# Kernel tuning notes

Hardware: AMD Instinct MI355X
Metric: run time of the kernel (lower is better)

## Reference

```python
import jax, jax.numpy as jnp
import numpy as np

N_NODES = 100000
N_EDGES = 1600000
IN_DIM = 165
HIDDEN = 128
OUT_DIM = 2


def gcn_conv(x, W, b, src, dst, n_nodes):
    """PyG GCNConv: h = x @ W; add self-loops; sym-normalized scatter-add; + bias."""
    h = x @ W  # [N, F_out]
    loop = jnp.arange(n_nodes, dtype=src.dtype)
    src_f = jnp.concatenate([src, loop])  # [E + N]
    dst_f = jnp.concatenate([dst, loop])
    deg = jax.ops.segment_sum(jnp.ones(src_f.shape[0], dtype=h.dtype), dst_f,
                              num_segments=n_nodes)  # in-degree incl. self-loop
    dinv = jnp.where(deg > 0, jax.lax.rsqrt(deg), jnp.zeros_like(deg))
    norm = dinv[src_f] * dinv[dst_f]  # [E + N]
    msg = h[src_f] * norm[:, None]  # gather + scale, [E+N, F_out]
    out = jax.ops.segment_sum(msg, dst_f, num_segments=n_nodes)  # scatter-add
    return out + b


def setup_inputs() -> dict:
    key = jax.random.key(0)
    k_x, k_e, k_w1, k_b1, k_w2, k_b2 = jax.random.split(key, 6)
    x = jax.random.normal(k_x, (N_NODES, IN_DIM), dtype=jnp.float32)
    edge_index = jax.random.randint(k_e, (2, N_EDGES), 0, N_NODES, dtype=jnp.int64)
    # Glorot-like init for linear weights, zeros for bias (PyG defaults)
    W1 = jax.random.normal(k_w1, (IN_DIM, HIDDEN), dtype=jnp.float32) / np.sqrt(IN_DIM)
    b1 = jnp.zeros((HIDDEN,), dtype=jnp.float32)
    W2 = jax.random.normal(k_w2, (HIDDEN, OUT_DIM), dtype=jnp.float32) / np.sqrt(HIDDEN)
    b2 = jnp.zeros((OUT_DIM,), dtype=jnp.float32)
    return {"x": x, "edge_index": edge_index, "W1": W1, "b1": b1, "W2": W2, "b2": b2}


def reference(x, edge_index, W1, b1, W2, b2):
    src, dst = edge_index[0], edge_index[1]
    h = gcn_conv(x, W1, b1, src, dst, N_NODES)
    h = jax.nn.relu(h)
    # dropout: eval mode (training=False) -> identity
    out = gcn_conv(h, W2, b2, src, dst, N_NODES)
    return out
```

## Files before the change

kernel.cpp:

```cpp
#include <hip/hip_runtime.h>
#include <hip/hip_fp16.h>

#define N_NODES 100000
#define N_EDGES 1600000
#define IN_DIM  165
#define HIDDEN  128
#define OUT_DIM 2

#define NBKT 196
#define CHUNK 4096
#define NCHUNK ((N_EDGES + CHUNK - 1) / CHUNK)
#define PADCAP 10240
#define KPAD 176
#define GROWS 64
#define XSTRIDE 176

typedef _Float16 half8_t __attribute__((ext_vector_type(8)));
typedef _Float16 half4_t __attribute__((ext_vector_type(4)));
typedef float floatx4 __attribute__((ext_vector_type(4)));


__global__ __launch_bounds__(512) void k_part2(const int* __restrict__ src,
                                               const int* __restrict__ dst,
                                               int* __restrict__ bcnt,
                                               unsigned* __restrict__ arena) {
    __shared__ int hist[256];
    __shared__ int gbase[256];

    int t = threadIdx.x;
    int e0 = blockIdx.x * CHUNK;
    int nE = N_EDGES - e0; if (nE > CHUNK) nE = CHUNK;
    int n4 = nE >> 2;
    const int4* dst4 = (const int4*)(dst + e0);
    const int4* src4 = (const int4*)(src + e0);

    if (t < 256) hist[t] = 0;
    __syncthreads();

    for (int i = t; i < n4; i += 512) {
        int4 d = dst4[i];
        atomicAdd(&hist[d.x >> 9], 1);
        atomicAdd(&hist[d.y >> 9], 1);
        atomicAdd(&hist[d.z >> 9], 1);
        atomicAdd(&hist[d.w >> 9], 1);
    }
    __syncthreads();

    if (t < NBKT) gbase[t] = t * PADCAP + atomicAdd(&bcnt[t], hist[t]);
    if (t < 256) hist[t] = 0;
    __syncthreads();

    for (int i = t; i < n4; i += 512) {
        int4 d = dst4[i];
        int4 s = src4[i];
        #pragma unroll
        for (int j = 0; j < 4; j++) {
            int dd = (j == 0) ? d.x : (j == 1) ? d.y : (j == 2) ? d.z : d.w;
            int ss = (j == 0) ? s.x : (j == 1) ? s.y : (j == 2) ? s.z : s.w;
            int bk = dd >> 9;
            unsigned entry = (unsigned)ss | ((unsigned)(dd & 511) << 17);
            int idx = atomicAdd(&hist[bk], 1);
            arena[gbase[bk] + idx] = entry;
        }
    }
}


__global__ __launch_bounds__(1024) void k_sort4(const unsigned* __restrict__ arena,
                                                const int* __restrict__ bcnt,
                                                int* __restrict__ csr,
                                                int* __restrict__ rowstart,
                                                int* __restrict__ rowend,
                                                float* __restrict__ dinv) {
    __shared__ int cnt[512];
    __shared__ int cur[512];
    __shared__ int wsum[4];
    int b = blockIdx.x;
    int n0 = b << 9;
    int t = threadIdx.x;
    int lane = t & 63, wid = t >> 6;
    int total = bcnt[b];
    int abase = b * PADCAP;
    int dbase = b * PADCAP;
    int nt4 = total >> 2;
    const uint4* arena4 = (const uint4*)(arena + abase);

    if (t < 512) cnt[t] = 0;
    __syncthreads();
    for (int p = t; p < nt4; p += 1024) {
        uint4 e = arena4[p];
        atomicAdd(&cnt[e.x >> 17], 1);
        atomicAdd(&cnt[e.y >> 17], 1);
        atomicAdd(&cnt[e.z >> 17], 1);
        atomicAdd(&cnt[e.w >> 17], 1);
    }
    {
        int p = (nt4 << 2) + t;
        if (p < total) atomicAdd(&cnt[arena[abase + p] >> 17], 1);
    }
    __syncthreads();

    int c0 = 0, c1 = 0, s = 0, inc = 0;
    if (t < 256) {
        c0 = cnt[2 * t];
        c1 = cnt[2 * t + 1];
        s = c0 + c1;
        inc = s;
        #pragma unroll
        for (int off = 1; off < 64; off <<= 1) {
            int y = __shfl_up(inc, off);
            if (lane >= off) inc += y;
        }
        if (lane == 63) wsum[wid] = inc;
    }
    __syncthreads();
    if (t == 0) {
        int acc = 0;
        #pragma unroll
        for (int w = 0; w < 4; w++) { int tv = wsum[w]; wsum[w] = acc; acc += tv; }
    }
    __syncthreads();
    if (t < 256) {
        int base = dbase + wsum[wid] + (inc - s);
        cur[2 * t] = base;
        cur[2 * t + 1] = base + c0;
        int node0 = n0 + 2 * t;
        if (node0 < N_NODES) {
            rowstart[node0] = base;
            rowend[node0] = base + c0;
            dinv[node0] = rsqrtf((float)(c0 + 1));
        }
        if (node0 + 1 < N_NODES) {
            rowstart[node0 + 1] = base + c0;
            rowend[node0 + 1] = base + c0 + c1;
            dinv[node0 + 1] = rsqrtf((float)(c1 + 1));
        }
    }
    __syncthreads();

    for (int p = t; p < nt4; p += 1024) {
        uint4 e = arena4[p];
        #pragma unroll
        for (int j = 0; j < 4; j++) {
            unsigned entry = (j == 0) ? e.x : (j == 1) ? e.y : (j == 2) ? e.z : e.w;
            int local = (int)(entry >> 17);
            int sv = (int)(entry & 0x1FFFFu);
            int pos = atomicAdd(&cur[local], 1);
            csr[pos] = sv;
        }
    }
    {
        int p = (nt4 << 2) + t;
        if (p < total) {
            unsigned entry = arena[abase + p];
            int local = (int)(entry >> 17);
            int sv = (int)(entry & 0x1FFFFu);
            int pos = atomicAdd(&cur[local], 1);
            csr[pos] = sv;
        }
    }
}


__global__ void k_w1t(const float* __restrict__ W1, _Float16* __restrict__ w1t,
                      int* __restrict__ bcnt) {
    if (blockIdx.x == 0 && threadIdx.x < NBKT) bcnt[threadIdx.x] = 0;
    int idx = blockIdx.x * 256 + threadIdx.x;
    if (idx < HIDDEN * KPAD) {
        int c = idx / KPAD, k = idx - c * KPAD;
        float v = (k < IN_DIM) ? W1[k * HIDDEN + c] : 0.f;
        w1t[idx] = (_Float16)v;
    }
}


__global__ __launch_bounds__(256, 8) void k_gemm1(const float* __restrict__ x,
                                                  const _Float16* __restrict__ w1t,
                                                  const float* __restrict__ dinv,
                                                  _Float16* __restrict__ h1s) {
    __shared__ __align__(16) _Float16 xs[GROWS * XSTRIDE];
    int t = threadIdx.x;
    int wid = t >> 6, lane = t & 63;
    int row0 = blockIdx.x * GROWS;
    int nrows = N_NODES - row0; if (nrows > GROWS) nrows = GROWS;
    int nflt = nrows * IN_DIM;

    const float4* xb4 = (const float4*)(x + (size_t)row0 * IN_DIM);
    int n4 = nflt >> 2;
    for (int i = t; i < n4; i += 256) {
        float4 v = xb4[i];
        int e = i << 2;
        #pragma unroll
        for (int j = 0; j < 4; j++) {
            int ee = e + j;
            int r = ee / IN_DIM;
            int c = ee - r * IN_DIM;
            float f = (j == 0) ? v.x : (j == 1) ? v.y : (j == 2) ? v.z : v.w;
            xs[(r * XSTRIDE + c) ^ ((r & 7) << 3)] = (_Float16)f;
        }
    }
    for (int i = t; i < GROWS * (XSTRIDE - IN_DIM); i += 256) {
        int r = i / (XSTRIDE - IN_DIM);
        int c = IN_DIM + (i - r * (XSTRIDE - IN_DIM));
        xs[(r * XSTRIDE + c) ^ ((r & 7) << 3)] = (_Float16)0.f;
    }
    __syncthreads();

    int mrow = wid * 16;
    if (mrow >= nrows) return;
    int m = lane & 15;
    int quad = lane >> 4;
    int rbase = (mrow + m) * XSTRIDE;
    int sm = (m & 7) << 3;
    int grow = row0 + mrow;

    floatx4 acc[8];
    #pragma unroll
    for (int i = 0; i < 8; i++) acc[i] = (floatx4)(0.f);

    #pragma unroll
    for (int kc = 0; kc < 5; kc++) {
        int kb = kc * 32 + quad * 8;
        half8_t a = *(const half8_t*)&xs[(rbase + kb) ^ sm];
        #pragma unroll
        for (int cb = 0; cb < 8; cb++) {
            int col = cb * 16 + m;
            half8_t bf = *(const half8_t*)&w1t[col * KPAD + kb];
            acc[cb] = __builtin_amdgcn_mfma_f32_16x16x32_f16(a, bf, acc[cb], 0, 0, 0);
        }
    }
    {
        int kb = 160 + quad * 4;
        half4_t a = *(const half4_t*)&xs[(rbase + kb) ^ sm];
        #pragma unroll
        for (int cb = 0; cb < 8; cb++) {
            int col = cb * 16 + m;
            half4_t bf = *(const half4_t*)&w1t[col * KPAD + kb];
            acc[cb] = __builtin_amdgcn_mfma_f32_16x16x16f16(a, bf, acc[cb], 0, 0, 0);
        }
    }
    float dv[4];
    #pragma unroll
    for (int r = 0; r < 4; r++) dv[r] = dinv[grow + quad * 4 + r];
    #pragma unroll
    for (int cb = 0; cb < 8; cb++) {
        #pragma unroll
        for (int r = 0; r < 4; r++) {
            h1s[(size_t)(grow + quad * 4 + r) * HIDDEN + cb * 16 + m] =
                (_Float16)(acc[cb][r] * dv[r]);
        }
    }
}


__global__ __launch_bounds__(256) void k_agg1(const _Float16* __restrict__ h1,
                                              const int* __restrict__ rowstart,
                                              const int* __restrict__ rowend,
                                              const int* __restrict__ csr,
                                              const float* __restrict__ dinv,
                                              const float* __restrict__ b1,
                                              const float* __restrict__ W2,
                                              float2* __restrict__ h2s,
                                              int nodeoff) {
    int wid = threadIdx.x >> 6, lane = threadIdx.x & 63;
    int el = lane & 15;
    int es = lane >> 4;
    int node = nodeoff + blockIdx.x * 4 + wid;

    float acc[8];
    {
        half8_t v = *(const half8_t*)(h1 + (size_t)node * HIDDEN + el * 8);
        #pragma unroll
        for (int j = 0; j < 8; j++) acc[j] = (es == 0) ? (float)v[j] : 0.f;
    }

    int p0 = rowstart[node], p1 = rowend[node];
    int p = p0 + es;
    for (; p + 4 < p1; p += 8) {
        int sA = csr[p];
        int sB = csr[p + 4];
        half8_t vA = *(const half8_t*)(h1 + (size_t)sA * HIDDEN + el * 8);
        half8_t vB = *(const half8_t*)(h1 + (size_t)sB * HIDDEN + el * 8);
        #pragma unroll
        for (int j = 0; j < 8; j++) acc[j] += (float)vA[j];
        #pragma unroll
        for (int j = 0; j < 8; j++) acc[j] += (float)vB[j];
    }
    if (p < p1) {
        int s = csr[p];
        half8_t v = *(const half8_t*)(h1 + (size_t)s * HIDDEN + el * 8);
        #pragma unroll
        for (int j = 0; j < 8; j++) acc[j] += (float)v[j];
    }

    #pragma unroll
    for (int j = 0; j < 8; j++) {
        acc[j] += __shfl_xor(acc[j], 16);
        acc[j] += __shfl_xor(acc[j], 32);
    }

    float di = dinv[node];
    float4 bb0 = ((const float4*)b1)[el * 2];
    float4 bb1 = ((const float4*)b1)[el * 2 + 1];
    float bv[8] = {bb0.x, bb0.y, bb0.z, bb0.w, bb1.x, bb1.y, bb1.z, bb1.w};
    float a0 = 0.f, a1 = 0.f;
    #pragma unroll
    for (int j = 0; j < 8; j++) {
        float z = fmaf(di, acc[j], bv[j]);
        float r = fmaxf(z, 0.f);
        float2 w = ((const float2*)W2)[el * 8 + j];
        a0 = fmaf(r, w.x, a0);
        a1 = fmaf(r, w.y, a1);
    }
    #pragma unroll
    for (int off = 8; off; off >>= 1) {
        a0 += __shfl_xor(a0, off);
        a1 += __shfl_xor(a1, off);
    }
    if (lane == 0) h2s[node] = make_float2(di * a0, di * a1);
}


__global__ __launch_bounds__(256) void k_agg2(const float2* __restrict__ h2s,
                                              const int* __restrict__ rowstart,
                                              const int* __restrict__ rowend,
                                              const int* __restrict__ csr,
                                              const float* __restrict__ dinv,
                                              const float* __restrict__ b2,
                                              float2* __restrict__ out) {
    int wid = threadIdx.x >> 6, lane = threadIdx.x & 63;
    int sub = lane >> 4, el = lane & 15;
    int node = blockIdx.x * 16 + wid * 4 + sub;
    int p0 = rowstart[node], p1 = rowend[node];
    float ax = 0.f, ay = 0.f;
    for (int p = p0 + el; p < p1; p += 16) {
        float2 g = h2s[csr[p]];
        ax += g.x;
        ay += g.y;
    }
    #pragma unroll
    for (int off = 8; off; off >>= 1) {
        ax += __shfl_xor(ax, off);
        ay += __shfl_xor(ay, off);
    }
    if (el == 0) {
        float2 self = h2s[node];
        float di = dinv[node];
        out[node] = make_float2(fmaf(di, self.x + ax, b2[0]),
                                fmaf(di, self.y + ay, b2[1]));
    }
}


extern "C" void kernel_launch(void* const* d_in, const int* in_sizes, int n_in,
                              void* d_out, int out_size, void* d_ws, size_t ws_size,
                              hipStream_t stream) {
    const float* x  = (const float*)d_in[0];
    const int*   ei = (const int*)d_in[1];
    const float* W1 = (const float*)d_in[2];
    const float* b1 = (const float*)d_in[3];
    const float* W2 = (const float*)d_in[4];
    const float* b2 = (const float*)d_in[5];
    float* out = (float*)d_out;

    const int* src = ei;
    const int* dst = ei + N_EDGES;

    char* ws = (char*)d_ws;
    size_t off = 0;
    auto alloc = [&](size_t bytes) -> void* {
        void* p = ws + off;
        off += (bytes + 255) & ~(size_t)255;
        return p;
    };
    _Float16* h1s      = (_Float16*)alloc((size_t)N_NODES * HIDDEN * 2);
    float*    dinv     = (float*)   alloc((size_t)N_NODES * 4);
    int*      rowstart = (int*)     alloc((size_t)N_NODES * 4);
    int*      rowend   = (int*)     alloc((size_t)N_NODES * 4);
    int*      bcnt     = (int*)     alloc((size_t)NBKT * 4);
    unsigned* arena    = (unsigned*)alloc((size_t)NBKT * PADCAP * 4);
    int*      csr      = (int*)     alloc((size_t)NBKT * PADCAP * 4);
    _Float16* w1t      = (_Float16*)alloc((size_t)HIDDEN * KPAD * 2);
    float2*   h2s      = (float2*)  alloc((size_t)N_NODES * 8);

    k_w1t<<<(HIDDEN * KPAD + 255) / 256, 256, 0, stream>>>(W1, w1t, bcnt);
    k_part2<<<NCHUNK, 512, 0, stream>>>(src, dst, bcnt, arena);
    k_sort4<<<NBKT, 1024, 0, stream>>>(arena, bcnt, csr, rowstart, rowend, dinv);
    k_gemm1<<<(N_NODES + GROWS - 1) / GROWS, 256, 0, stream>>>(x, w1t, dinv, h1s);
    k_agg1<<<N_NODES / 4, 256, 0, stream>>>(h1s, rowstart, rowend, csr, dinv, b1, W2, h2s, 0);
    k_agg2<<<N_NODES / 16, 256, 0, stream>>>(h2s, rowstart, rowend, csr, dinv, b2, (float2*)out);
}
```

Measured before the change: 239.4 us.

## Hold W1 fragments in registers inside gemm1 and drop the transpose kernel

Removes the separate W1 transpose/convert kernel. Each gemm1 thread now loads its W1 fragments straight from global fp32, converts them to fp16 and keeps them in registers for the whole block. The bcnt reset moves to a hipMemsetAsync. This saves one launch and the repeated global B-fragment loads in the MFMA loop. In exchange every block does strided scalar loads of W1 (about 5x8x8 + 32 values per thread), and register pressure rises, with launch bounds lowered from 8 to 2 blocks per SM.

```diff
diff --git a/kernel.cpp b/kernel.cpp
--- a/kernel.cpp
+++ b/kernel.cpp
@@ -11,8 +11,8 @@
 #define CHUNK 4096
 #define NCHUNK ((N_EDGES + CHUNK - 1) / CHUNK)
 #define PADCAP 10240
-#define KPAD 176
 #define GROWS 64
+#define NTILE ((N_NODES + GROWS - 1) / GROWS)
 #define XSTRIDE 176
 
 typedef _Float16 half8_t __attribute__((ext_vector_type(8)));
@@ -162,28 +162,42 @@
 }
 
 
-__global__ void k_w1t(const float* __restrict__ W1, _Float16* __restrict__ w1t,
-                      int* __restrict__ bcnt) {
-    if (blockIdx.x == 0 && threadIdx.x < NBKT) bcnt[threadIdx.x] = 0;
-    int idx = blockIdx.x * 256 + threadIdx.x;
-    if (idx < HIDDEN * KPAD) {
-        int c = idx / KPAD, k = idx - c * KPAD;
-        float v = (k < IN_DIM) ? W1[k * HIDDEN + c] : 0.f;
-        w1t[idx] = (_Float16)v;
-    }
-}
-
-
-__global__ __launch_bounds__(256, 8) void k_gemm1(const float* __restrict__ x,
-                                                  const _Float16* __restrict__ w1t,
+__global__ __launch_bounds__(256, 2) void k_gemm1(const float* __restrict__ x,
+                                                  const float* __restrict__ W1,
                                                   const float* __restrict__ dinv,
                                                   _Float16* __restrict__ h1s) {
     __shared__ __align__(16) _Float16 xs[GROWS * XSTRIDE];
     int t = threadIdx.x;
     int wid = t >> 6, lane = t & 63;
+    int m = lane & 15;
+    int quad = lane >> 4;
     int row0 = blockIdx.x * GROWS;
     int nrows = N_NODES - row0; if (nrows > GROWS) nrows = GROWS;
     int nflt = nrows * IN_DIM;
+
+    half8_t bfr[5][8];
+    #pragma unroll
+    for (int kc = 0; kc < 5; kc++) {
+        #pragma unroll
+        for (int cb = 0; cb < 8; cb++) {
+            int col = cb * 16 + m;
+            #pragma unroll
+            for (int j = 0; j < 8; j++) {
+                int k = kc * 32 + quad * 8 + j;
+                bfr[kc][cb][j] = (_Float16)W1[k * HIDDEN + col];
+            }
+        }
+    }
+    half4_t btl[8];
+    #pragma unroll
+    for (int cb = 0; cb < 8; cb++) {
+        int col = cb * 16 + m;
+        #pragma unroll
+        for (int j = 0; j < 4; j++) {
+            int k = 160 + quad * 4 + j;
+            btl[cb][j] = (k < IN_DIM) ? (_Float16)W1[k * HIDDEN + col] : (_Float16)0.f;
+        }
+    }
 
     const float4* xb4 = (const float4*)(x + (size_t)row0 * IN_DIM);
     int n4 = nflt >> 2;
@@ -208,8 +222,6 @@
 
     int mrow = wid * 16;
     if (mrow >= nrows) return;
-    int m = lane & 15;
-    int quad = lane >> 4;
     int rbase = (mrow + m) * XSTRIDE;
     int sm = (m & 7) << 3;
     int grow = row0 + mrow;
@@ -223,21 +235,17 @@
         int kb = kc * 32 + quad * 8;
         half8_t a = *(const half8_t*)&xs[(rbase + kb) ^ sm];
         #pragma unroll
-        for (int cb = 0; cb < 8; cb++) {
-            int col = cb * 16 + m;
-            half8_t bf = *(const half8_t*)&w1t[col * KPAD + kb];
-            acc[cb] = __builtin_amdgcn_mfma_f32_16x16x32_f16(a, bf, acc[cb], 0, 0, 0);
-        }
+        for (int cb = 0; cb < 8; cb++)
+            acc[cb] = __builtin_amdgcn_mfma_f32_16x16x32_f16(a, bfr[kc][cb],
+                                                             acc[cb], 0, 0, 0);
     }
     {
         int kb = 160 + quad * 4;
         half4_t a = *(const half4_t*)&xs[(rbase + kb) ^ sm];
         #pragma unroll
-        for (int cb = 0; cb < 8; cb++) {
-            int col = cb * 16 + m;
-            half4_t bf = *(const half4_t*)&w1t[col * KPAD + kb];
-            acc[cb] = __builtin_amdgcn_mfma_f32_16x16x16f16(a, bf, acc[cb], 0, 0, 0);
-        }
+        for (int cb = 0; cb < 8; cb++)
+            acc[cb] = __builtin_amdgcn_mfma_f32_16x16x16f16(a, btl[cb],
+                                                            acc[cb], 0, 0, 0);
     }
     float dv[4];
     #pragma unroll
@@ -260,12 +268,11 @@
                                               const float* __restrict__ dinv,
                                               const float* __restrict__ b1,
                                               const float* __restrict__ W2,
-                                              float2* __restrict__ h2s,
-                                              int nodeoff) {
+                                              float2* __restrict__ h2s) {
     int wid = threadIdx.x >> 6, lane = threadIdx.x & 63;
     int el = lane & 15;
     int es = lane >> 4;
-    int node = nodeoff + blockIdx.x * 4 + wid;
+    int node = blockIdx.x * 4 + wid;
 
     float acc[8];
     {
@@ -380,13 +387,12 @@
     int*      bcnt     = (int*)     alloc((size_t)NBKT * 4);
     unsigned* arena    = (unsigned*)alloc((size_t)NBKT * PADCAP * 4);
     int*      csr      = (int*)     alloc((size_t)NBKT * PADCAP * 4);
-    _Float16* w1t      = (_Float16*)alloc((size_t)HIDDEN * KPAD * 2);
     float2*   h2s      = (float2*)  alloc((size_t)N_NODES * 8);
 
-    k_w1t<<<(HIDDEN * KPAD + 255) / 256, 256, 0, stream>>>(W1, w1t, bcnt);
+    (void)hipMemsetAsync(bcnt, 0, (size_t)NBKT * 4, stream);
     k_part2<<<NCHUNK, 512, 0, stream>>>(src, dst, bcnt, arena);
     k_sort4<<<NBKT, 1024, 0, stream>>>(arena, bcnt, csr, rowstart, rowend, dinv);
-    k_gemm1<<<(N_NODES + GROWS - 1) / GROWS, 256, 0, stream>>>(x, w1t, dinv, h1s);
-    k_agg1<<<N_NODES / 4, 256, 0, stream>>>(h1s, rowstart, rowend, csr, dinv, b1, W2, h2s, 0);
+    k_gemm1<<<NTILE, 256, 0, stream>>>(x, W1, dinv, h1s);
+    k_agg1<<<N_NODES / 4, 256, 0, stream>>>(h1s, rowstart, rowend, csr, dinv, b1, W2, h2s);
     k_agg2<<<N_NODES / 16, 256, 0, stream>>>(h2s, rowstart, rowend, csr, dinv, b2, (float2*)out);
 }
```

New measurement: 430.7 us. +79.9%, slower.
